# Performance work log

Hardware: AMD Instinct MI355X
Metric: run time of the kernel (lower is better)

The kernel has to match this reference:

```python
import jax, jax.numpy as jnp
import numpy as np

B, N, IN_C, OUT_C, H, M, E = 1, 20000, 256, 64, 4, 30, 320000
EPS = 1e-6


def _projection_matrix(m, d, seed=0):
    # NodeFormer create_projection_matrix: stacked transposed-QR blocks, rows
    # rescaled by norms of iid gaussian rows (scaling=0).
    rng = np.random.RandomState(seed)
    blocks = []
    nb_full = m // d
    for _ in range(nb_full):
        q, _ = np.linalg.qr(rng.randn(d, d))
        blocks.append(q.T)
    rem = m - nb_full * d
    if rem > 0:
        q, _ = np.linalg.qr(rng.randn(d, d))
        blocks.append(q.T[:rem])
    final = np.vstack(blocks)
    multiplier = np.linalg.norm(rng.randn(m, d), axis=1)
    return jnp.asarray(multiplier[:, None] * final, dtype=jnp.float32)


def _linear(key, out_f, in_f):
    k1, k2 = jax.random.split(key)
    s = 1.0 / np.sqrt(in_f)
    w = jax.random.uniform(k1, (out_f, in_f), jnp.float32, -s, s)
    b = jax.random.uniform(k2, (out_f,), jnp.float32, -s, s)
    return w, b


def setup_inputs() -> dict:
    key = jax.random.key(0)
    ks = jax.random.split(key, 8)
    Wq_w, Wq_b = _linear(ks[3], H * OUT_C, IN_C)
    Wk_w, Wk_b = _linear(ks[4], H * OUT_C, IN_C)
    Wv_w, Wv_b = _linear(ks[5], H * OUT_C, IN_C)
    Wo_w, Wo_b = _linear(ks[6], OUT_C, H * OUT_C)
    return {
        'z': jax.random.normal(ks[0], (B, N, IN_C), jnp.float32),
        'feat': jax.random.normal(ks[1], (B, N, IN_C), jnp.float32),
        'edge_index': jax.random.randint(ks[2], (2, E), 0, N),
        'tau': jnp.asarray(0.25, jnp.float32),
        'Wq_w': Wq_w, 'Wq_b': Wq_b,
        'Wk_w': Wk_w, 'Wk_b': Wk_b,
        'Wv_w': Wv_w, 'Wv_b': Wv_b,
        'Wo_w': Wo_w, 'Wo_b': Wo_b,
        'b_param': jnp.full((1, H), 0.1, jnp.float32),  # rb_order=1, sigmoid init
        'proj': _projection_matrix(M, OUT_C),
    }


def _softmax_kernel(x, proj, is_query):
    # Performer positive softmax kernel feature map. x: [B,N,H,D] -> [B,N,H,M]
    d = x.shape[-1]
    x = x * (float(d) ** -0.25)
    ratio = 1.0 / jnp.sqrt(jnp.asarray(proj.shape[0], x.dtype))
    xd = jnp.einsum('bnhd,md->bnhm', x, proj)
    diag = 0.5 * jnp.sum(x * x, axis=-1, keepdims=True)
    if is_query:
        mx = jnp.max(xd, axis=-1, keepdims=True)
    else:
        mx = jnp.max(jnp.max(xd, axis=-1, keepdims=True), axis=1, keepdims=True)
    return ratio * (jnp.exp(xd - diag - mx) + EPS)


def reference(z, feat, edge_index, tau, Wq_w, Wq_b, Wk_w, Wk_b, Wv_w, Wv_b,
              Wo_w, Wo_b, b_param, proj):
    Bn, Nn = z.shape[0], z.shape[1]
    q = (feat @ Wq_w.T + Wq_b).reshape(Bn, Nn, H, OUT_C)
    k = (feat @ Wk_w.T + Wk_b).reshape(Bn, Nn, H, OUT_C)
    v = (z @ Wv_w.T + Wv_b).reshape(Bn, Nn, H, OUT_C)

    inv = 1.0 / jnp.sqrt(tau)
    qp = _softmax_kernel(q * inv, proj, True)    # [B,N,H,M]
    kp = _softmax_kernel(k * inv, proj, False)   # [B,N,H,M]

    # Linear (kernelized) attention, O(N*H*M*D)
    kvs = jnp.einsum('bnhm,bnhd->bhmd', kp, v)
    num = jnp.einsum('bnhm,bhmd->bnhd', qp, kvs)
    den = jnp.einsum('bnhm,bhm->bnh', qp, jnp.sum(kp, axis=1))[..., None]
    z_next = num / den                            # [B,N,H,D]

    # Relational bias: GCN-style normalized scatter with per-head scalar weight
    row, col = edge_index[0], edge_index[1]
    d_in = jnp.zeros((Nn,), z.dtype).at[col].add(1.0)
    d_out = jnp.zeros((Nn,), z.dtype).at[row].add(1.0)
    edge_w = jnp.nan_to_num(jnp.sqrt(1.0 / d_in[col]) * jnp.sqrt(1.0 / d_out[row]),
                            nan=0.0, posinf=0.0, neginf=0.0)    # [E]
    msgs = v[:, row] * edge_w[None, :, None, None]              # [B,E,H,D]
    agg = jnp.zeros_like(v).at[:, col].add(msgs)                # [B,N,H,D]
    z_next = z_next + jax.nn.sigmoid(b_param[0])[None, None, :, None] * agg

    out = z_next.reshape(Bn, Nn, H * OUT_C) @ Wo_w.T + Wo_b     # [B,N,OUT_C]
    return out
```

## Files before the change

kernel.cpp:

```cpp
#include <hip/hip_runtime.h>

#define NN 20000
#define EE 320000
#define RATIO_F 0.18257418583505536f
#define EPS_F 1e-6f
#define SCALE_D4 0.35355339059327373f
#define NCH 157

typedef _Float16 f16x8 __attribute__((ext_vector_type(8)));
typedef _Float16 f16x4 __attribute__((ext_vector_type(4)));
typedef float f32x4 __attribute__((ext_vector_type(4)));

__device__ __forceinline__ unsigned fenc(float x) {
  unsigned u = __float_as_uint(x);
  return (u & 0x80000000u) ? ~u : (u | 0x80000000u);
}
__device__ __forceinline__ float fdec(unsigned u) {
  return (u & 0x80000000u) ? __uint_as_float(u & 0x7FFFFFFFu) : __uint_as_float(~u);
}
__device__ __forceinline__ void fma4(float* a, float s, float4 b) {
  a[0] = fmaf(s, b.x, a[0]);
  a[1] = fmaf(s, b.y, a[1]);
  a[2] = fmaf(s, b.z, a[2]);
  a[3] = fmaf(s, b.w, a[3]);
}
__device__ __forceinline__ void gload16(const void* g, void* l) {
  __builtin_amdgcn_global_load_lds(
      (const __attribute__((address_space(1))) unsigned int*)g,
      (__attribute__((address_space(3))) unsigned int*)l, 16, 0, 0);
}

__global__ __launch_bounds__(256)
void k0_build(const float* __restrict__ Wq, const float* __restrict__ Wk,
              const float* __restrict__ Wv, const float* __restrict__ bq,
              const float* __restrict__ bk, const float* __restrict__ bv,
              const float* __restrict__ proj, const float* __restrict__ tau,
              const float* __restrict__ Wo,
              _Float16* __restrict__ Wf, float* __restrict__ bbig,
              _Float16* __restrict__ WoFh, _Float16* __restrict__ WoFl) {
  const int blk = blockIdx.x;
  const int i = threadIdx.x;
  const int kt = i >> 5, gg = (i >> 3) & 3, j = i & 7;
  if (blk >= 1024) {
    const int col = blk - 1024;
    const float val = Wo[col * 256 + i];
    const int lane = gg * 16 + (col & 15);
    const size_t off = (size_t)((col >> 4) * 8 + kt) * 512 + lane * 8 + j;
    const _Float16 hb = (_Float16)val;
    WoFh[off] = hb;
    WoFl[off] = (_Float16)(val - (float)hb);
    return;
  }
  const int col = blk;
  const float s = rsqrtf(tau[0]) * SCALE_D4;
  float val = 0.f, bias = 0.f;
  if (col < 256) {
    val = Wq[col * 256 + i]; bias = bq[col];
  } else if (col < 512) {
    const int c = col - 256;
    val = Wk[c * 256 + i]; bias = bk[c];
  } else if (col < 768) {
    const int c = col - 512;
    val = Wv[c * 256 + i]; bias = bv[c];
  } else {
    const int rr = col - 768;
    const int grp = rr >> 7;
    const int h = (rr >> 5) & 3, m = rr & 31;
    if (m < 30) {
      const float* W = grp ? Wk : Wq;
      const float* bb = grp ? bk : bq;
      float a = 0.f, ba = 0.f;
#pragma unroll 8
      for (int d = 0; d < 64; ++d) {
        const float pr = proj[m * 64 + d];
        a  = fmaf(pr, W[(h * 64 + d) * 256 + i], a);
        ba = fmaf(pr, bb[h * 64 + d], ba);
      }
      val = s * a; bias = s * ba;
    }
  }
  const int lane = gg * 16 + (col & 15);
  const size_t off = (size_t)((col >> 4) * 8 + kt) * 512 + lane * 8 + j;
  Wf[off] = (_Float16)val;
  if (i == 0) bbig[col] = bias;
}

__device__ __forceinline__ void cvt_half(const float4* raw, f16x8* Ah, f16x8* Al) {
#pragma unroll
  for (int kt = 0; kt < 4; ++kt) {
    const float ff[8] = {raw[kt*2].x, raw[kt*2].y, raw[kt*2].z, raw[kt*2].w,
                         raw[kt*2+1].x, raw[kt*2+1].y, raw[kt*2+1].z, raw[kt*2+1].w};
    union { _Float16 h[8]; f16x8 v; } hu, lu;
#pragma unroll
    for (int j = 0; j < 8; ++j) {
      const _Float16 hb = (_Float16)ff[j];
      hu.h[j] = hb;
      lu.h[j] = (_Float16)(ff[j] - (float)hb);
    }
    Ah[kt] = hu.v; Al[kt] = lu.v;
  }
}

__device__ __forceinline__ int ct_of(int s, int isv, int h, int y) {
  if (isv) return 32 + (y - 4) * 8 + s;
  if (s < 4)  return h * 4 + s;
  if (s < 8)  return 16 + h * 4 + (s - 4);
  if (s < 10) return 48 + 2 * h + (s - 8);
  return 56 + 2 * h + (s - 10);
}

__global__ __launch_bounds__(512, 4)
void k1_all(const float* __restrict__ feat, const float* __restrict__ zin,
            const _Float16* __restrict__ Wf, const float* __restrict__ bbig,
            const float* __restrict__ tau,
            _Float16* __restrict__ qph, float* __restrict__ kbuf,
            _Float16* __restrict__ vh, unsigned* __restrict__ kmaxU) {
  __shared__ __align__(16) _Float16 blds[12 * 2048];
  const int t = threadIdx.x;
  const int wid = t >> 6, lane = t & 63;
  const int g = lane >> 4, cl = lane & 15;
  const int y = blockIdx.y;
  const int h = y & 3;
  const int rbase = blockIdx.x * 128 + wid * 16;
  int arow = rbase + cl; if (arow > NN - 1) arow = NN - 1;

  if (y < 4) {
    const float* arp = feat + (size_t)arow * 256;
#pragma unroll
    for (int r = 0; r < 6; ++r) {
      const int idx = r * 4096 + t * 8;
      const int s = idx >> 11, wi = idx & 2047;
      gload16(Wf + (size_t)ct_of(s, 0, h, y) * 4096 + wi, &blds[idx]);
    }
    float4 raw[8];
#pragma unroll
    for (int l = 0; l < 4; ++l) {
      raw[l * 2]     = *(const float4*)(arp + l * 32 + g * 8);
      raw[l * 2 + 1] = *(const float4*)(arp + l * 32 + g * 8 + 4);
    }
    f16x8 Ah[4], Al[4];
    cvt_half(raw, Ah, Al);
    __syncthreads();
#pragma unroll
    for (int l = 0; l < 4; ++l) {
      raw[l * 2]     = *(const float4*)(arp + (l + 4) * 32 + g * 8);
      raw[l * 2 + 1] = *(const float4*)(arp + (l + 4) * 32 + g * 8 + 4);
    }
    f32x4 acc[12];
#pragma unroll
    for (int s = 0; s < 12; ++s) acc[s] = (f32x4){0.f, 0.f, 0.f, 0.f};
#pragma unroll
    for (int ktl = 0; ktl < 4; ++ktl) {
#pragma unroll
      for (int s = 0; s < 12; ++s) {
        const f16x8 b = *(const f16x8*)&blds[s * 2048 + ktl * 512 + lane * 8];
        acc[s] = __builtin_amdgcn_mfma_f32_16x16x32_f16(Ah[ktl], b, acc[s], 0, 0, 0);
        acc[s] = __builtin_amdgcn_mfma_f32_16x16x32_f16(Al[ktl], b, acc[s], 0, 0, 0);
      }
    }
    __syncthreads();
#pragma unroll
    for (int r = 0; r < 6; ++r) {
      const int idx = r * 4096 + t * 8;
      const int s = idx >> 11, wi = idx & 2047;
      gload16(Wf + (size_t)ct_of(s, 0, h, y) * 4096 + 2048 + wi, &blds[idx]);
    }
    cvt_half(raw, Ah, Al);
    __syncthreads();
#pragma unroll
    for (int ktl = 0; ktl < 4; ++ktl) {
#pragma unroll
      for (int s = 0; s < 12; ++s) {
        const f16x8 b = *(const f16x8*)&blds[s * 2048 + ktl * 512 + lane * 8];
        acc[s] = __builtin_amdgcn_mfma_f32_16x16x32_f16(Ah[ktl], b, acc[s], 0, 0, 0);
        acc[s] = __builtin_amdgcn_mfma_f32_16x16x32_f16(Al[ktl], b, acc[s], 0, 0, 0);
      }
    }
#pragma unroll
    for (int s = 0; s < 12; ++s) {
      const float bb = bbig[ct_of(s, 0, h, y) * 16 + cl];
#pragma unroll
      for (int j = 0; j < 4; ++j) acc[s][j] += bb;
    }
    const float sc = rsqrtf(tau[0]) * SCALE_D4;
    const float h2 = 0.5f * sc * sc;
    float dsq[4], dsk[4];
#pragma unroll
    for (int j = 0; j < 4; ++j) {
      dsq[j] = acc[0][j] * acc[0][j] + acc[1][j] * acc[1][j] +
               acc[2][j] * acc[2][j] + acc[3][j] * acc[3][j];
      dsk[j] = acc[4][j] * acc[4][j] + acc[5][j] * acc[5][j] +
               acc[6][j] * acc[6][j] + acc[7][j] * acc[7][j];
    }
#pragma unroll
    for (int m = 1; m < 16; m <<= 1) {
#pragma unroll
      for (int j = 0; j < 4; ++j) {
        dsq[j] += __shfl_xor(dsq[j], m);
        dsk[j] += __shfl_xor(dsk[j], m);
      }
    }
    {
#pragma unroll
      for (int j = 0; j < 4; ++j) {
        const float x0 = acc[8][j], x1 = acc[9][j];
        float mv = fmaxf(x0, (cl < 14) ? x1 : -3.4e38f);
#pragma unroll
        for (int m = 1; m < 16; m <<= 1) mv = fmaxf(mv, __shfl_xor(mv, m));
        const float dg = h2 * dsq[j];
        const int r = rbase + 4 * g + j;
        if (r < NN) {
          _Float16* dst = qph + (size_t)r * 120 + h * 30;
          dst[cl] = (_Float16)(RATIO_F * (expf(x0 - dg - mv) + EPS_F));
          if (cl < 14)
            dst[16 + cl] = (_Float16)(RATIO_F * (expf(x1 - dg - mv) + EPS_F));
        }
      }
    }
    {
      float wmax = -3.4e38f;
#pragma unroll
      for (int j = 0; j < 4; ++j) {
        const float x0 = acc[10][j], x1 = acc[11][j];
        float mv = fmaxf(x0, (cl < 14) ? x1 : -3.4e38f);
#pragma unroll
        for (int m = 1; m < 16; m <<= 1) mv = fmaxf(mv, __shfl_xor(mv, m));
        wmax = fmaxf(wmax, mv);
        const float dg = h2 * dsk[j];
        const int r = rbase + 4 * g + j;
        if (r < NN) {
          float* dst = kbuf + (size_t)r * 120 + h * 30;
          dst[cl] = x0 - dg;
          if (cl < 14) dst[16 + cl] = x1 - dg;
        }
      }
      wmax = fmaxf(wmax, __shfl_xor(wmax, 16));
      wmax = fmaxf(wmax, __shfl_xor(wmax, 32));
      if (lane == 0) atomicMax(&kmaxU[h], fenc(wmax));
    }
  } else {
    const float* arp = zin + (size_t)arow * 256;
#pragma unroll
    for (int r = 0; r < 4; ++r) {
      const int idx = r * 4096 + t * 8;
      const int s = idx >> 11, wi = idx & 2047;
      gload16(Wf + (size_t)ct_of(s, 1, h, y) * 4096 + wi, &blds[idx]);
    }
    float4 raw[8];
#pragma unroll
    for (int l = 0; l < 4; ++l) {
      raw[l * 2]     = *(const float4*)(arp + l * 32 + g * 8);
      raw[l * 2 + 1] = *(const float4*)(arp + l * 32 + g * 8 + 4);
    }
    f16x8 Ah[4], Al[4];
    cvt_half(raw, Ah, Al);
    __syncthreads();
#pragma unroll
    for (int l = 0; l < 4; ++l) {
      raw[l * 2]     = *(const float4*)(arp + (l + 4) * 32 + g * 8);
      raw[l * 2 + 1] = *(const float4*)(arp + (l + 4) * 32 + g * 8 + 4);
    }
    f32x4 acc[8];
#pragma unroll
    for (int s = 0; s < 8; ++s) acc[s] = (f32x4){0.f, 0.f, 0.f, 0.f};
#pragma unroll
    for (int ktl = 0; ktl < 4; ++ktl) {
#pragma unroll
      for (int s = 0; s < 8; ++s) {
        const f16x8 b = *(const f16x8*)&blds[s * 2048 + ktl * 512 + lane * 8];
        acc[s] = __builtin_amdgcn_mfma_f32_16x16x32_f16(Ah[ktl], b, acc[s], 0, 0, 0);
        acc[s] = __builtin_amdgcn_mfma_f32_16x16x32_f16(Al[ktl], b, acc[s], 0, 0, 0);
      }
    }
    __syncthreads();
#pragma unroll
    for (int r = 0; r < 4; ++r) {
      const int idx = r * 4096 + t * 8;
      const int s = idx >> 11, wi = idx & 2047;
      gload16(Wf + (size_t)ct_of(s, 1, h, y) * 4096 + 2048 + wi, &blds[idx]);
    }
    cvt_half(raw, Ah, Al);
    __syncthreads();
#pragma unroll
    for (int ktl = 0; ktl < 4; ++ktl) {
#pragma unroll
      for (int s = 0; s < 8; ++s) {
        const f16x8 b = *(const f16x8*)&blds[s * 2048 + ktl * 512 + lane * 8];
        acc[s] = __builtin_amdgcn_mfma_f32_16x16x32_f16(Ah[ktl], b, acc[s], 0, 0, 0);
        acc[s] = __builtin_amdgcn_mfma_f32_16x16x32_f16(Al[ktl], b, acc[s], 0, 0, 0);
      }
    }
#pragma unroll
    for (int s = 0; s < 8; ++s) {
      const int ct = ct_of(s, 1, h, y);
      const float bb = bbig[ct * 16 + cl];
      const int colb = (ct - 32) * 16 + cl;
#pragma unroll
      for (int j = 0; j < 4; ++j) {
        const int r = rbase + 4 * g + j;
        if (r < NN) vh[(size_t)r * 256 + colb] = (_Float16)(acc[s][j] + bb);
      }
    }
  }
}

__global__ __launch_bounds__(256)
void k3_kvs(const float* __restrict__ kbr, const _Float16* __restrict__ vh,
            const unsigned* __restrict__ kmaxU, float* __restrict__ partial) {
  __shared__ float kpch[128 * 32];
  __shared__ float vch[128 * 68];
  const int h = blockIdx.y;
  const int n0 = blockIdx.x * 128;
  const int cnt = min(128, NN - n0);
  const int t = threadIdx.x;
  const float mx = fdec(kmaxU[h]);
  const int m = t >> 3, dg = t & 7, d0 = dg * 8;
#pragma unroll
  for (int l = 0; l < 15; ++l) {
    const int flat = l * 256 + t;
    const int nl = flat / 30, mm = flat - nl * 30;
    kpch[nl * 32 + mm] = (nl < cnt)
        ? RATIO_F * (expf(kbr[(size_t)(n0 + nl) * 120 + h * 30 + mm] - mx) + EPS_F)
        : 0.f;
  }
#pragma unroll
  for (int l = 0; l < 8; ++l) {
    const int f4 = l * 256 + t;
    const int nl = f4 >> 4, dd = (f4 & 15) * 4;
    float4 vv = make_float4(0.f, 0.f, 0.f, 0.f);
    if (nl < cnt) {
      f16x4 u = *(const f16x4*)(vh + (size_t)(n0 + nl) * 256 + h * 64 + dd);
      vv = make_float4((float)u[0], (float)u[1], (float)u[2], (float)u[3]);
    }
    *(float4*)&vch[nl * 68 + dd] = vv;
  }
  __syncthreads();
  float acc[8] = {0, 0, 0, 0, 0, 0, 0, 0};
  float asum = 0.f;
  const int ms = (m < 30) ? m : 0;
  for (int nl = 0; nl < cnt; ++nl) {
    const float kv = kpch[nl * 32 + ms];
    const float4 va = *(const float4*)&vch[nl * 68 + d0];
    const float4 vb = *(const float4*)&vch[nl * 68 + d0 + 4];
    fma4(&acc[0], kv, va);
    fma4(&acc[4], kv, vb);
    asum += kv;
  }
  if (m < 30) {
    float* dst = partial + ((size_t)blockIdx.y * NCH + blockIdx.x) * 1952 + m * 64 + d0;
#pragma unroll
    for (int j = 0; j < 8; ++j) dst[j] = acc[j];
    if (dg == 0)
      partial[((size_t)blockIdx.y * NCH + blockIdx.x) * 1952 + 1920 + m] = asum;
  }
}

__global__ __launch_bounds__(256)
void k3b_reduce(const float* __restrict__ partial, float* __restrict__ kvs,
                float* __restrict__ ksum) {
  const int idx = blockIdx.x * 256 + threadIdx.x;
  if (idx >= 4 * 1952) return;
  const int h = idx / 1952, q = idx - h * 1952;
  float s = 0.f;
  for (int c = 0; c < NCH; ++c)
    s += partial[((size_t)h * NCH + c) * 1952 + q];
  if (q < 1920) kvs[h * 1920 + q] = s;
  else if (q < 1950) ksum[h * 30 + (q - 1920)] = s;
}

__global__ __launch_bounds__(256)
void k4_attn(const _Float16* __restrict__ qph, const float* __restrict__ kvs,
             const float* __restrict__ ksum, const _Float16* __restrict__ aggh,
             const float* __restrict__ bp, _Float16* __restrict__ zh) {
  __shared__ float kvsl[120 * 68];
  __shared__ float ksl[120];
  __shared__ float qpl[32 * 120];
  const int t = threadIdx.x;
  const int n0 = blockIdx.x * 32;
#pragma unroll
  for (int l = 0; l < 30; ++l) {
    const int f = l * 256 + t;
    const int hm = f >> 6, d = f & 63;
    kvsl[hm * 68 + d] = kvs[f];
  }
  if (t < 120) ksl[t] = ksum[t];
#pragma unroll
  for (int l = 0; l < 15; ++l) {
    const int f = l * 256 + t;
    qpl[f] = (float)qph[(size_t)n0 * 120 + f];
  }
  __syncthreads();
  const int nl = t >> 3, dg = t & 7, d0 = dg * 8;
  const float* qrow = &qpl[nl * 120];
  float den[4] = {0, 0, 0, 0};
  for (int m = 0; m < 30; ++m) {
#pragma unroll
    for (int hh = 0; hh < 4; ++hh) den[hh] = fmaf(qrow[hh * 30 + m], ksl[hh * 30 + m], den[hh]);
  }
  float acc[4][8] = {};
  for (int m = 0; m < 30; ++m) {
#pragma unroll
    for (int hh = 0; hh < 4; ++hh) {
      const float qv = qrow[hh * 30 + m];
      const float* kr = &kvsl[(hh * 30 + m) * 68 + d0];
      const float4 ka = *(const float4*)kr;
      const float4 kb = *(const float4*)(kr + 4);
      fma4(&acc[hh][0], qv, ka);
      fma4(&acc[hh][4], qv, kb);
    }
  }
  const size_t n = n0 + nl;
#pragma unroll
  for (int hh = 0; hh < 4; ++hh) {
    const float inv = 1.0f / den[hh];
    const float sg = 1.f / (1.f + expf(-bp[hh]));
    const f16x8 ag = *(const f16x8*)(aggh + n * 256 + hh * 64 + d0);
    f16x8 o;
#pragma unroll
    for (int jj = 0; jj < 8; ++jj)
      o[jj] = (_Float16)(acc[hh][jj] * inv + sg * (float)ag[jj]);
    *(f16x8*)(zh + n * 256 + hh * 64 + d0) = o;
  }
}

__global__ __launch_bounds__(256)
void k5_deg(const int* __restrict__ ei, int* __restrict__ dini, int* __restrict__ douti) {
  const int q = blockIdx.x * 256 + threadIdx.x;
  if (q >= EE / 4) return;
  const int4 r4 = *(const int4*)(ei + q * 4);
  const int4 c4 = *(const int4*)(ei + EE + q * 4);
  atomicAdd(&dini[c4.x], 1); atomicAdd(&dini[c4.y], 1);
  atomicAdd(&dini[c4.z], 1); atomicAdd(&dini[c4.w], 1);
  atomicAdd(&douti[r4.x], 1); atomicAdd(&douti[r4.y], 1);
  atomicAdd(&douti[r4.z], 1); atomicAdd(&douti[r4.w], 1);
}

__global__ __launch_bounds__(1024)
void k6a_scan(const int* __restrict__ cnt, int* __restrict__ off) {
  __shared__ int s[1024];
  const int t = threadIdx.x;
  int4 v[5];
  int sum = 0;
  const int4* p4 = (const int4*)(cnt + t * 20);
#pragma unroll
  for (int i = 0; i < 5; ++i) {
    v[i] = p4[i];
    sum += v[i].x + v[i].y + v[i].z + v[i].w;
  }
  s[t] = sum;
  __syncthreads();
  for (int o = 1; o < 1024; o <<= 1) {
    const int add = (t >= o) ? s[t - o] : 0;
    __syncthreads();
    s[t] += add;
    __syncthreads();
  }
  int run = (t == 0) ? 0 : s[t - 1];
  if (t == 0) off[0] = 0;
  const int base = t * 20;
#pragma unroll
  for (int i = 0; i < 5; ++i) {
    const int vals[4] = {v[i].x, v[i].y, v[i].z, v[i].w};
#pragma unroll
    for (int j = 0; j < 4; ++j) {
      const int idx = base + i * 4 + j;
      if (idx < NN) { run += vals[j]; off[idx + 1] = run; }
    }
  }
}

__global__ __launch_bounds__(256)
void k6bc(const int* __restrict__ ei, const int* __restrict__ coff,
          int* __restrict__ cursor, int* __restrict__ crow,
          const int* __restrict__ douti, float* __restrict__ rw) {
  const int b = blockIdx.x;
  if (b < EE / 256) {
    const int e = b * 256 + threadIdx.x;
    const int r = ei[e], c = ei[EE + e];
    const int pos = atomicAdd(&cursor[c], 1);
    crow[coff[c] + pos] = r;
  } else {
    const int n = (b - EE / 256) * 256 + threadIdx.x;
    if (n < NN) rw[n] = rsqrtf((float)douti[n]);
  }
}

__global__ __launch_bounds__(256)
void k7g_gather(const int* __restrict__ coff, const int* __restrict__ crow,
                const float* __restrict__ rw, const _Float16* __restrict__ vh,
                _Float16* __restrict__ aggh) {
  const int node = blockIdx.x * 4 + (threadIdx.x >> 6);
  const int lane = threadIdx.x & 63;
  const int o0 = coff[node], o1 = coff[node + 1];
  float a0 = 0.f, a1 = 0.f, a2 = 0.f, a3 = 0.f;
  if (o1 > o0) {
    int e = o0;
    for (; e + 8 <= o1; e += 8) {
      int rr[8];
#pragma unroll
      for (int u = 0; u < 8; ++u) rr[u] = crow[e + u];
      float ww[8];
#pragma unroll
      for (int u = 0; u < 8; ++u) ww[u] = rw[rr[u]];
#pragma unroll
      for (int u = 0; u < 8; ++u) {
        const f16x4 vv = *(const f16x4*)(vh + (size_t)rr[u] * 256 + lane * 4);
        a0 = fmaf(ww[u], (float)vv[0], a0);
        a1 = fmaf(ww[u], (float)vv[1], a1);
        a2 = fmaf(ww[u], (float)vv[2], a2);
        a3 = fmaf(ww[u], (float)vv[3], a3);
      }
    }
    for (; e < o1; ++e) {
      const int r = crow[e];
      const float wr = rw[r];
      const f16x4 vv = *(const f16x4*)(vh + (size_t)r * 256 + lane * 4);
      a0 = fmaf(wr, (float)vv[0], a0);
      a1 = fmaf(wr, (float)vv[1], a1);
      a2 = fmaf(wr, (float)vv[2], a2);
      a3 = fmaf(wr, (float)vv[3], a3);
    }
    const float rin = rsqrtf((float)(o1 - o0));
    a0 *= rin; a1 *= rin; a2 *= rin; a3 *= rin;
  }
  f16x4 st;
  st[0] = (_Float16)a0; st[1] = (_Float16)a1;
  st[2] = (_Float16)a2; st[3] = (_Float16)a3;
  *(f16x4*)(aggh + (size_t)node * 256 + lane * 4) = st;
}

__global__ __launch_bounds__(512, 4)
void k8m_out(const _Float16* __restrict__ zh, const _Float16* __restrict__ WoFh,
             const _Float16* __restrict__ WoFl, const float* __restrict__ bo,
             float* __restrict__ out) {
  __shared__ __align__(16) _Float16 blds[8 * 4096];
  const int t = threadIdx.x;
  const int wid = t >> 6, lane = t & 63;
  const int g = lane >> 4, cl = lane & 15;
  const int rbase = blockIdx.x * 128 + wid * 16;
  int arow = rbase + cl; if (arow > NN - 1) arow = NN - 1;
#pragma unroll
  for (int s = 0; s < 4; ++s) {
    gload16(WoFh + (size_t)s * 4096 + t * 8, &blds[(s * 512 + t) * 8]);
    gload16(WoFl + (size_t)s * 4096 + t * 8, &blds[((s + 4) * 512 + t) * 8]);
  }
  const _Float16* zr = zh + (size_t)arow * 256;
  f16x8 Ah[8];
#pragma unroll
  for (int kt = 0; kt < 8; ++kt)
    Ah[kt] = *(const f16x8*)(zr + kt * 32 + g * 8);
  __syncthreads();
  f32x4 acc[4];
#pragma unroll
  for (int s = 0; s < 4; ++s) acc[s] = (f32x4){0.f, 0.f, 0.f, 0.f};
#pragma unroll
  for (int kt = 0; kt < 8; ++kt) {
#pragma unroll
    for (int s = 0; s < 4; ++s) {
      const f16x8 bh = *(const f16x8*)&blds[s * 4096 + kt * 512 + lane * 8];
      const f16x8 bl = *(const f16x8*)&blds[(s + 4) * 4096 + kt * 512 + lane * 8];
      acc[s] = __builtin_amdgcn_mfma_f32_16x16x32_f16(Ah[kt], bh, acc[s], 0, 0, 0);
      acc[s] = __builtin_amdgcn_mfma_f32_16x16x32_f16(Ah[kt], bl, acc[s], 0, 0, 0);
    }
  }
#pragma unroll
  for (int s = 0; s < 4; ++s) {
    const float bb = bo[s * 16 + cl];
#pragma unroll
    for (int j = 0; j < 4; ++j) {
      const int r = rbase + 4 * g + j;
      if (r < NN) out[(size_t)r * 64 + s * 16 + cl] = acc[s][j] + bb;
    }
  }
}

extern "C" void kernel_launch(void* const* d_in, const int* in_sizes, int n_in,
                              void* d_out, int out_size, void* d_ws, size_t ws_size,
                              hipStream_t stream) {
  (void)in_sizes; (void)n_in; (void)out_size; (void)ws_size;
  const float* z    = (const float*)d_in[0];
  const float* feat = (const float*)d_in[1];
  const int*   ei   = (const int*)d_in[2];
  const float* tau  = (const float*)d_in[3];
  const float* Wq_w = (const float*)d_in[4];
  const float* Wq_b = (const float*)d_in[5];
  const float* Wk_w = (const float*)d_in[6];
  const float* Wk_b = (const float*)d_in[7];
  const float* Wv_w = (const float*)d_in[8];
  const float* Wv_b = (const float*)d_in[9];
  const float* Wo_w = (const float*)d_in[10];
  const float* Wo_b = (const float*)d_in[11];
  const float* bp   = (const float*)d_in[12];
  const float* proj = (const float*)d_in[13];
  float* out = (float*)d_out;

  char* p = (char*)d_ws;
  auto alloc = [&](size_t bytes) { char* r = p; p += (bytes + 255) & ~(size_t)255; return r; };
  _Float16* Wf    = (_Float16*)alloc((size_t)256 * 1024 * 2);
  _Float16* WoFh  = (_Float16*)alloc((size_t)64 * 256 * 2);
  _Float16* WoFl  = (_Float16*)alloc((size_t)64 * 256 * 2);
  float*    bbig  = (float*)alloc(1024 * 4);
  _Float16* vh    = (_Float16*)alloc((size_t)NN * 256 * 2);
  _Float16* aggh  = (_Float16*)alloc((size_t)NN * 256 * 2);
  _Float16* qph   = (_Float16*)alloc((size_t)NN * 120 * 2);
  float*    kbuf  = (float*)alloc((size_t)NN * 120 * 4);
  _Float16* zh    = (_Float16*)alloc((size_t)NN * 256 * 2);
  float*    partial = (float*)alloc((size_t)4 * NCH * 1952 * 4);
  float*    kvs   = (float*)alloc(7680 * 4);
  float*    ksum  = (float*)alloc(120 * 4);
  float*    rw    = (float*)alloc((size_t)NN * 4);
  char* z0 = p;
  unsigned* kmaxU = (unsigned*)alloc(16);
  int*      dini  = (int*)alloc((size_t)20480 * 4);
  int*      douti = (int*)alloc((size_t)NN * 4);
  int*      cursor= (int*)alloc((size_t)NN * 4);
  char* z1 = p;
  int*      coff  = (int*)alloc((size_t)(NN + 1) * 4);
  int*      crow  = (int*)alloc((size_t)EE * 4);

  hipMemsetAsync(z0, 0, (size_t)(z1 - z0), stream);

  k0_build<<<1088, 256, 0, stream>>>(Wq_w, Wk_w, Wv_w, Wq_b, Wk_b, Wv_b, proj,
                                     tau, Wo_w, Wf, bbig, WoFh, WoFl);
  k5_deg<<<(EE / 4 + 255) / 256, 256, 0, stream>>>(ei, dini, douti);
  k6a_scan<<<1, 1024, 0, stream>>>(dini, coff);
  k6bc<<<EE / 256 + (NN + 255) / 256, 256, 0, stream>>>(ei, coff, cursor, crow,
                                                        douti, rw);
  k1_all<<<dim3(157, 6), 512, 0, stream>>>(feat, z, Wf, bbig, tau, qph, kbuf, vh, kmaxU);
  k7g_gather<<<NN / 4, 256, 0, stream>>>(coff, crow, rw, vh, aggh);
  k3_kvs<<<dim3(NCH, 4), 256, 0, stream>>>(kbuf, vh, kmaxU, partial);
  k3b_reduce<<<(4 * 1952 + 255) / 256, 256, 0, stream>>>(partial, kvs, ksum);
  k4_attn<<<NN / 32, 256, 0, stream>>>(qph, kvs, ksum, aggh, bp, zh);
  k8m_out<<<157, 512, 0, stream>>>(zh, WoFh, WoFl, Wo_b, out);
}
```

Before: 257.2 us.

## Fuse degree count into build kernel, deepen gather unroll, split output GEMM across waves

The edge-degree atomic counting moves into extra blocks of the weight-build kernel, which removes one launch and lets that work overlap with the weight packing. The gather loop is unrolled to 16 edges with a 4-edge tail so more independent loads are in flight per wave. The output projection kernel now gives each wave one 16-column tile instead of all four. That uses 628 blocks instead of 157 to fill more CUs, at the cost of each block reloading the full Wo tiles into LDS for fewer rows.

Result: no change. 257.2 us (+0.0%).

```diff
diff --git a/kernel.cpp b/kernel.cpp
--- a/kernel.cpp
+++ b/kernel.cpp
@@ -35,11 +35,24 @@
               const float* __restrict__ Wv, const float* __restrict__ bq,
               const float* __restrict__ bk, const float* __restrict__ bv,
               const float* __restrict__ proj, const float* __restrict__ tau,
-              const float* __restrict__ Wo,
+              const float* __restrict__ Wo, const int* __restrict__ ei,
               _Float16* __restrict__ Wf, float* __restrict__ bbig,
-              _Float16* __restrict__ WoFh, _Float16* __restrict__ WoFl) {
+              _Float16* __restrict__ WoFh, _Float16* __restrict__ WoFl,
+              int* __restrict__ dini, int* __restrict__ douti) {
   const int blk = blockIdx.x;
   const int i = threadIdx.x;
+  if (blk >= 1088) {
+    const int q = (blk - 1088) * 256 + i;
+    if (q < EE / 4) {
+      const int4 r4 = *(const int4*)(ei + q * 4);
+      const int4 c4 = *(const int4*)(ei + EE + q * 4);
+      atomicAdd(&dini[c4.x], 1); atomicAdd(&dini[c4.y], 1);
+      atomicAdd(&dini[c4.z], 1); atomicAdd(&dini[c4.w], 1);
+      atomicAdd(&douti[r4.x], 1); atomicAdd(&douti[r4.y], 1);
+      atomicAdd(&douti[r4.z], 1); atomicAdd(&douti[r4.w], 1);
+    }
+    return;
+  }
   const int kt = i >> 5, gg = (i >> 3) & 3, j = i & 7;
   if (blk >= 1024) {
     const int col = blk - 1024;
@@ -423,18 +436,6 @@
   }
 }
 
-__global__ __launch_bounds__(256)
-void k5_deg(const int* __restrict__ ei, int* __restrict__ dini, int* __restrict__ douti) {
-  const int q = blockIdx.x * 256 + threadIdx.x;
-  if (q >= EE / 4) return;
-  const int4 r4 = *(const int4*)(ei + q * 4);
-  const int4 c4 = *(const int4*)(ei + EE + q * 4);
-  atomicAdd(&dini[c4.x], 1); atomicAdd(&dini[c4.y], 1);
-  atomicAdd(&dini[c4.z], 1); atomicAdd(&dini[c4.w], 1);
-  atomicAdd(&douti[r4.x], 1); atomicAdd(&douti[r4.y], 1);
-  atomicAdd(&douti[r4.z], 1); atomicAdd(&douti[r4.w], 1);
-}
-
 __global__ __launch_bounds__(1024)
 void k6a_scan(const int* __restrict__ cnt, int* __restrict__ off) {
   __shared__ int s[1024];
@@ -495,15 +496,31 @@
   float a0 = 0.f, a1 = 0.f, a2 = 0.f, a3 = 0.f;
   if (o1 > o0) {
     int e = o0;
-    for (; e + 8 <= o1; e += 8) {
-      int rr[8];
-#pragma unroll
-      for (int u = 0; u < 8; ++u) rr[u] = crow[e + u];
-      float ww[8];
-#pragma unroll
-      for (int u = 0; u < 8; ++u) ww[u] = rw[rr[u]];
-#pragma unroll
-      for (int u = 0; u < 8; ++u) {
+    for (; e + 16 <= o1; e += 16) {
+      int rr[16];
+#pragma unroll
+      for (int u = 0; u < 16; ++u) rr[u] = crow[e + u];
+      float ww[16];
+#pragma unroll
+      for (int u = 0; u < 16; ++u) ww[u] = rw[rr[u]];
+#pragma unroll
+      for (int u = 0; u < 16; ++u) {
+        const f16x4 vv = *(const f16x4*)(vh + (size_t)rr[u] * 256 + lane * 4);
+        a0 = fmaf(ww[u], (float)vv[0], a0);
+        a1 = fmaf(ww[u], (float)vv[1], a1);
+        a2 = fmaf(ww[u], (float)vv[2], a2);
+        a3 = fmaf(ww[u], (float)vv[3], a3);
+      }
+    }
+    for (; e + 4 <= o1; e += 4) {
+      int rr[4];
+#pragma unroll
+      for (int u = 0; u < 4; ++u) rr[u] = crow[e + u];
+      float ww[4];
+#pragma unroll
+      for (int u = 0; u < 4; ++u) ww[u] = rw[rr[u]];
+#pragma unroll
+      for (int u = 0; u < 4; ++u) {
         const f16x4 vv = *(const f16x4*)(vh + (size_t)rr[u] * 256 + lane * 4);
         a0 = fmaf(ww[u], (float)vv[0], a0);
         a1 = fmaf(ww[u], (float)vv[1], a1);
@@ -537,7 +554,8 @@
   const int t = threadIdx.x;
   const int wid = t >> 6, lane = t & 63;
   const int g = lane >> 4, cl = lane & 15;
-  const int rbase = blockIdx.x * 128 + wid * 16;
+  const int rt = wid >> 2, ct = wid & 3;
+  const int rbase = blockIdx.x * 32 + rt * 16;
   int arow = rbase + cl; if (arow > NN - 1) arow = NN - 1;
 #pragma unroll
   for (int s = 0; s < 4; ++s) {
@@ -550,27 +568,19 @@
   for (int kt = 0; kt < 8; ++kt)
     Ah[kt] = *(const f16x8*)(zr + kt * 32 + g * 8);
   __syncthreads();
-  f32x4 acc[4];
-#pragma unroll
-  for (int s = 0; s < 4; ++s) acc[s] = (f32x4){0.f, 0.f, 0.f, 0.f};
+  f32x4 acc = {0.f, 0.f, 0.f, 0.f};
 #pragma unroll
   for (int kt = 0; kt < 8; ++kt) {
-#pragma unroll
-    for (int s = 0; s < 4; ++s) {
-      const f16x8 bh = *(const f16x8*)&blds[s * 4096 + kt * 512 + lane * 8];
-      const f16x8 bl = *(const f16x8*)&blds[(s + 4) * 4096 + kt * 512 + lane * 8];
-      acc[s] = __builtin_amdgcn_mfma_f32_16x16x32_f16(Ah[kt], bh, acc[s], 0, 0, 0);
-      acc[s] = __builtin_amdgcn_mfma_f32_16x16x32_f16(Ah[kt], bl, acc[s], 0, 0, 0);
-    }
-  }
-#pragma unroll
-  for (int s = 0; s < 4; ++s) {
-    const float bb = bo[s * 16 + cl];
-#pragma unroll
-    for (int j = 0; j < 4; ++j) {
-      const int r = rbase + 4 * g + j;
-      if (r < NN) out[(size_t)r * 64 + s * 16 + cl] = acc[s][j] + bb;
-    }
+    const f16x8 bh = *(const f16x8*)&blds[ct * 4096 + kt * 512 + lane * 8];
+    const f16x8 bl = *(const f16x8*)&blds[(ct + 4) * 4096 + kt * 512 + lane * 8];
+    acc = __builtin_amdgcn_mfma_f32_16x16x32_f16(Ah[kt], bh, acc, 0, 0, 0);
+    acc = __builtin_amdgcn_mfma_f32_16x16x32_f16(Ah[kt], bl, acc, 0, 0, 0);
+  }
+  const float bb = bo[ct * 16 + cl];
+#pragma unroll
+  for (int j = 0; j < 4; ++j) {
+    const int r = rbase + 4 * g + j;
+    if (r < NN) out[(size_t)r * 64 + ct * 16 + cl] = acc[j] + bb;
   }
 }
 
@@ -620,9 +630,9 @@
 
   hipMemsetAsync(z0, 0, (size_t)(z1 - z0), stream);
 
-  k0_build<<<1088, 256, 0, stream>>>(Wq_w, Wk_w, Wv_w, Wq_b, Wk_b, Wv_b, proj,
-                                     tau, Wo_w, Wf, bbig, WoFh, WoFl);
-  k5_deg<<<(EE / 4 + 255) / 256, 256, 0, stream>>>(ei, dini, douti);
+  k0_build<<<1088 + (EE / 4 + 255) / 256, 256, 0, stream>>>(
+      Wq_w, Wk_w, Wv_w, Wq_b, Wk_b, Wv_b, proj, tau, Wo_w, ei,
+      Wf, bbig, WoFh, WoFl, dini, douti);
   k6a_scan<<<1, 1024, 0, stream>>>(dini, coff);
   k6bc<<<EE / 256 + (NN + 255) / 256, 256, 0, stream>>>(ei, coff, cursor, crow,
                                                         douti, rw);
@@ -631,5 +641,5 @@
   k3_kvs<<<dim3(NCH, 4), 256, 0, stream>>>(kbuf, vh, kmaxU, partial);
   k3b_reduce<<<(4 * 1952 + 255) / 256, 256, 0, stream>>>(partial, kvs, ksum);
   k4_attn<<<NN / 32, 256, 0, stream>>>(qph, kvs, ksum, aggh, bp, zh);
-  k8m_out<<<157, 512, 0, stream>>>(zh, WoFh, WoFl, Wo_b, out);
-}
+  k8m_out<<<628, 512, 0, stream>>>(zh, WoFh, WoFl, Wo_b, out);
+}
```
